# Kernel optimization log

Hardware: AMD Instinct MI355X
Metric: run time of the kernel (lower is better)

Reference implementation:

```python
import jax, jax.numpy as jnp
import numpy as np
from jax.scipy.special import gammaln

B, N, F, K = 128, 29, 64, 64
MAXZ, NITER, NPATH = 56, 2, 20
CUTOFF = 5.0


def setup_inputs() -> dict:
    key = jax.random.key(0)
    ks = jax.random.split(key, 16)
    atomic_numbers = jax.random.randint(ks[0], (B, N), 1, MAXZ)
    positions = jax.random.normal(ks[1], (B, N, 3), dtype=jnp.float32) * 2.0
    Ef = jax.random.normal(ks[2], (B, 3), dtype=jnp.float32)
    # fully connected molecular graph (all ordered pairs i != j), E = N*(N-1) = 812
    ii, jj = np.meshgrid(np.arange(N), np.arange(N), indexing="ij")
    m = ii != jj
    dst_idx = jnp.asarray(ii[m], dtype=jnp.int32)
    src_idx = jnp.asarray(jj[m], dtype=jnp.int32)
    s = 1.0 / np.sqrt(F)
    t = 0.2  # tensor-product path weight scale (keeps activations bounded)
    return {
        "atomic_numbers": atomic_numbers, "positions": positions, "Ef": Ef,
        "dst_idx": dst_idx, "src_idx": src_idx,
        "embed": jax.random.normal(ks[3], (MAXZ, F), dtype=jnp.float32) * s,
        "mp_basis_w": jax.random.normal(ks[4], (NITER, K, F), dtype=jnp.float32) / np.sqrt(K),
        "mp_tp_w": jax.random.normal(ks[5], (NITER, NPATH, F), dtype=jnp.float32) * t,
        "d1_w": jax.random.normal(ks[6], (NITER, 2, 2, F, F), dtype=jnp.float32) * s,
        "d1_b": jnp.zeros((NITER, 2, F), dtype=jnp.float32),
        "d2_w": jax.random.normal(ks[7], (NITER, 2, 2, F, F), dtype=jnp.float32) * s,
        "d2_b": jnp.zeros((NITER, 2, F), dtype=jnp.float32),
        "tens_w": jax.random.normal(ks[8], (NITER, NPATH, F), dtype=jnp.float32) * t,
        "td_dense_w": jax.random.normal(ks[9], (NITER, 2, 2, F, F), dtype=jnp.float32) * s,
        "td_tp_w": jax.random.normal(ks[10], (NITER, NPATH, F), dtype=jnp.float32) * t,
        "out_w": jax.random.normal(ks[11], (F,), dtype=jnp.float32) * s,
        "element_bias": jax.random.normal(ks[12], (MAXZ,), dtype=jnp.float32) * 0.1,
    }


def _tp(a, b, w):
    """Channelwise Clebsch-Gordan tensor product for max_degree=1 with parity channels.
    a, b: (M, 2, 4, F) with axis1 = (regular, pseudo), axis2 = (l=0, l=1 x/y/z).
    w: (20, F) learned per-path weights (5 l-paths x 4 parity combos)."""
    M, Fd = a.shape[0], a.shape[-1]
    sr = jnp.zeros((M, Fd), a.dtype); sp = jnp.zeros((M, Fd), a.dtype)
    vr = jnp.zeros((M, 3, Fd), a.dtype); vp = jnp.zeros((M, 3, Fd), a.dtype)
    idx = 0
    for p1 in range(2):
        for p2 in range(2):
            s1 = a[:, p1, 0]; v1 = a[:, p1, 1:4]
            s2 = b[:, p2, 0]; v2 = b[:, p2, 1:4]
            pl0a = 1 - 2 * p1; pl0b = 1 - 2 * p2   # parity of l=0 slot
            pl1a = -(1 - 2 * p1); pl1b = -(1 - 2 * p2)  # parity of l=1 slot
            tt = w[idx] * s1 * s2
            if pl0a * pl0b == 1: sr = sr + tt
            else: sp = sp + tt
            tt = w[idx + 1] * s1[:, None, :] * v2
            if pl0a * pl1b == -1: vr = vr + tt
            else: vp = vp + tt
            tt = w[idx + 2] * v1 * s2[:, None, :]
            if pl1a * pl0b == -1: vr = vr + tt
            else: vp = vp + tt
            tt = w[idx + 3] * jnp.sum(v1 * v2, axis=1)
            if pl1a * pl1b == 1: sr = sr + tt
            else: sp = sp + tt
            tt = w[idx + 4] * jnp.cross(v1, v2, axis=1)
            if pl1a * pl1b == -1: vr = vr + tt
            else: vp = vp + tt
            idx += 5
    reg = jnp.concatenate([sr[:, None, :], vr], axis=1)
    pse = jnp.concatenate([sp[:, None, :], vp], axis=1)
    return jnp.stack([reg, pse], axis=1)  # (M, 2, 4, F)


def _dense(x, W, b=None):
    # per-(parity, degree) linear map over features; W: (2, 2, F, F), b: (2, F)
    s = jnp.einsum("npf,pfg->npg", x[:, :, 0, :], W[:, 0])
    v = jnp.einsum("npdf,pfg->npdg", x[:, :, 1:4, :], W[:, 1])
    if b is not None:
        s = s + b
    return jnp.concatenate([s[:, :, None, :], v], axis=2)


def _silu(x):
    # gated equivariant silu: silu on scalars, sigmoid(scalar) gate on vectors
    s = x[:, :, 0:1, :]
    g = jax.nn.sigmoid(s)
    return jnp.concatenate([s * g, x[:, :, 1:4, :] * g], axis=2)


def _radial(r):
    # reciprocal Bernstein radial basis with smooth cutoff
    k = jnp.arange(K, dtype=r.dtype)
    logc = gammaln(float(K)) - gammaln(k + 1.0) - gammaln(float(K) - k)
    u = 1.0 / (1.0 + r)
    logb = logc + k * jnp.log(u)[:, None] + (K - 1.0 - k) * jnp.log(jnp.maximum(1.0 - u, 1e-12))[:, None]
    x2 = (r / CUTOFF) ** 2
    fcut = jnp.where(x2 < 1.0, jnp.exp(1.0 - 1.0 / jnp.maximum(1.0 - x2, 1e-12)), 0.0)
    return jnp.exp(logb) * fcut[:, None]  # (E, K)


def reference(atomic_numbers, positions, Ef, dst_idx, src_idx, embed, mp_basis_w,
              mp_tp_w, d1_w, d1_b, d2_w, d2_b, tens_w, td_dense_w, td_tp_w,
              out_w, element_bias):
    Bsz, Nn = atomic_numbers.shape
    BN = Bsz * Nn
    Fd = embed.shape[-1]
    pos = positions.reshape(-1, 3)
    Z = atomic_numbers.reshape(-1)
    offsets = (jnp.arange(Bsz, dtype=dst_idx.dtype) * Nn)
    dstf = (dst_idx[None, :] + offsets[:, None]).reshape(-1)  # (B*E,)
    srcf = (src_idx[None, :] + offsets[:, None]).reshape(-1)
    disp = pos[srcf] - pos[dstf]                               # (B*E, 3)
    r = jnp.sqrt(jnp.sum(disp * disp, axis=-1) + 1e-12)
    unit = disp / r[:, None]
    sph = jnp.concatenate([jnp.ones_like(r)[:, None], unit], axis=-1)  # (B*E, 4)
    basis = sph[:, :, None] * _radial(r)[:, None, :]           # (B*E, 4, K)

    x = jnp.zeros((BN, 2, 4, Fd), dtype=positions.dtype)
    x = x.at[:, 0, 0, :].set(embed[Z])

    xEFv = jnp.concatenate([jnp.ones((Bsz, 1), positions.dtype), Ef], axis=-1)  # (B, 4)
    xEF = jnp.repeat(xEFv, Nn, axis=0)                          # (BN, 4)
    xEF = jnp.broadcast_to(xEF[:, None, :, None], (BN, 2, 4, Fd))

    for i in range(NITER):
        bproj = jnp.einsum("edk,kf->edf", basis, mp_basis_w[i])  # (B*E, 4, F)
        bfeat = jnp.stack([bproj, jnp.zeros_like(bproj)], axis=1)  # (B*E, 2, 4, F)
        msg = _tp(x[srcf], bfeat, mp_tp_w[i])
        if i == NITER - 1:  # last iteration: max_degree=0 messages
            msg = msg * jnp.array([1.0, 0.0, 0.0, 0.0], msg.dtype)[None, None, :, None]
        y = jax.ops.segment_sum(msg, dstf, num_segments=BN)
        x = x + y
        h = _dense(x, d1_w[i], d1_b[i])
        h = _silu(h)
        h = _dense(h, d2_w[i], d2_b[i])
        x = h + y
        x = x + _tp(x, xEF, tens_w[i])          # Tensor()(x, xEF)
        x = _tp(x, _dense(x, td_dense_w[i]), td_tp_w[i])  # TensorDense

    s = x[:, 0, 0, :]  # degree-0 regular channel
    atomic_energies = s @ out_w + element_bias[Z]
    energy = atomic_energies.reshape(Bsz, Nn).sum(axis=1)
    return energy
```

## Files before the change

kernel.cpp:

```cpp
#include <hip/hip_runtime.h>

#define NB 128
#define NA 29
#define BN (NB*NA)
#define FD 64
#define RPLANE (BN*28*64)


__global__ void prep_kernel(const float* __restrict__ d1b,
                            const float* __restrict__ d2b,
                            const float* __restrict__ d2w,
                            float* __restrict__ logc, float* __restrict__ c4,
                            float* __restrict__ out)
{
  const int t = threadIdx.x;
  if (t < 64) {
    logc[t] = lgammaf(64.0f) - lgammaf((float)t + 1.0f) - lgammaf(64.0f - (float)t);
  } else if (t < 128) {
    const int g = t - 64;
    float acc = d2b[64 + g];
    for (int f = 0; f < 64; ++f) {
      const float v  = d1b[64 + f];
      const float sv = v / (1.0f + expf(-v));
      acc += d2w[2*4096 + f*64 + g] * sv;
    }
    c4[g] = acc;
  } else {
    out[t - 128] = 0.0f;
  }
}

__global__ __launch_bounds__(256, 3) void edge_rproj_kernel(
    const float* __restrict__ pos,
    const float* __restrict__ Wb,
    const float* __restrict__ logc_tab,
    float* __restrict__ rp)
{
  __shared__ float elu[28], el1mu[28], efc[28];
  __shared__ float rads[28][FD];
  const int bn = blockIdx.x, b = bn / NA, n = bn - b*NA;
  const int tid = threadIdx.x, lane = tid & 63, wv = tid >> 6;

  if (tid < 28) {
    const int jr = tid, j = jr + (jr >= n ? 1 : 0);
    const float dx = pos[(b*NA+j)*3+0] - pos[(b*NA+n)*3+0];
    const float dy = pos[(b*NA+j)*3+1] - pos[(b*NA+n)*3+1];
    const float dz = pos[(b*NA+j)*3+2] - pos[(b*NA+n)*3+2];
    const float r  = sqrtf(dx*dx + dy*dy + dz*dz + 1e-12f);
    const float u  = 1.0f/(1.0f + r);
    elu[jr]   = logf(u);
    el1mu[jr] = logf(fmaxf(1.0f - u, 1e-12f));
    const float x2 = (r*0.2f)*(r*0.2f);
    efc[jr] = (x2 < 1.0f) ? expf(1.0f - 1.0f/fmaxf(1.0f - x2, 1e-12f)) : 0.0f;
  }
  const float kk   = (float)lane;
  const float logc = logc_tab[lane];
  __syncthreads();

  #pragma unroll
  for (int i = 0; i < 7; ++i) {
    const int e = wv*7 + i;
    rads[e][lane] = expf(logc + kk*elu[e] + (63.0f - kk)*el1mu[e]) * efc[e];
  }
  float wb[64];
  #pragma unroll
  for (int k = 0; k < 64; ++k) wb[k] = Wb[k*FD + lane];

  #pragma unroll
  for (int i = 0; i < 7; ++i) {
    const int jr = wv*7 + i;
    float a0 = 0.0f;
    #pragma unroll
    for (int k4 = 0; k4 < 16; ++k4) {
      const float4 rv = *(const float4*)&rads[jr][k4*4];
      a0 += wb[k4*4+0]*rv.x + wb[k4*4+1]*rv.y + wb[k4*4+2]*rv.z + wb[k4*4+3]*rv.w;
    }
    rp[((size_t)bn*28 + jr)*64 + lane] = a0;
  }
}

__global__ __launch_bounds__(512) void msg0_kernel(
    const int*   __restrict__ Z,
    const float* __restrict__ pos,
    const float* __restrict__ embed,
    const float* __restrict__ wtp,
    const float* __restrict__ rp,
    float* __restrict__ y)
{
  __shared__ float emb_sh[NA][FD];
  __shared__ float posb[NA][3];
  __shared__ float us_sh[8][28][3];
  const int bi = blockIdx.x, b = bi >> 2, shard = bi & 3;
  const int tid = threadIdx.x, r = tid >> 6, g = tid & 63;

  if (tid < NA) {
    posb[tid][0] = pos[(b*NA+tid)*3+0];
    posb[tid][1] = pos[(b*NA+tid)*3+1];
    posb[tid][2] = pos[(b*NA+tid)*3+2];
  }
  __syncthreads();
  for (int idx = tid; idx < NA*FD; idx += 512)
    emb_sh[idx>>6][idx&63] = embed[Z[b*NA + (idx>>6)]*FD + (idx&63)];
  if (tid < 224) {
    const int rr = tid/28, jr = tid - rr*28, nn = shard*8 + rr;
    if (nn < NA) {
      const int j = jr + (jr >= nn ? 1 : 0);
      const float dx = posb[j][0]-posb[nn][0];
      const float dy = posb[j][1]-posb[nn][1];
      const float dz = posb[j][2]-posb[nn][2];
      const float ri = 1.0f / sqrtf(dx*dx + dy*dy + dz*dz + 1e-12f);
      us_sh[rr][jr][0] = dx*ri; us_sh[rr][jr][1] = dy*ri; us_sh[rr][jr][2] = dz*ri;
    }
  }
  __syncthreads();

  const int n = shard*8 + r;
  if (n >= NA) return;
  const int bn = b*NA + n;
  const float wm0 = wtp[0*FD + g], wm1 = wtp[1*FD + g];

  float rpa[28];
  {
    const float* rpb = rp + (size_t)bn*28*64 + g;
    #pragma unroll
    for (int jr = 0; jr < 28; ++jr) rpa[jr] = rpb[jr*64];
  }
  float y0 = 0.0f, y1 = 0.0f, y2 = 0.0f, y3 = 0.0f;
  #pragma unroll
  for (int jr = 0; jr < 28; ++jr) {
    const int j = jr + (jr >= n ? 1 : 0);
    const float t0 = rpa[jr] * emb_sh[j][g];
    y0 += wm0*t0;
    const float t1 = wm1*t0;
    y1 += t1*us_sh[r][jr][0];
    y2 += t1*us_sh[r][jr][1];
    y3 += t1*us_sh[r][jr][2];
  }
  float* yb = y + (size_t)bn*256 + g;
  yb[0] = y0; yb[64] = y1; yb[128] = y2; yb[192] = y3;
}

__global__ __launch_bounds__(512) void msg1_kernel(
    const float* __restrict__ pos,
    const float* __restrict__ wtp,
    const float* __restrict__ rp,
    const float* __restrict__ x,
    float* __restrict__ y)
{
  __shared__ float x_sh[NA][8][FD];
  __shared__ float posb[NA][3];
  __shared__ float us_sh[8][28][3];
  const int bi = blockIdx.x, b = bi >> 2, shard = bi & 3;
  const int tid = threadIdx.x, r = tid >> 6, g = tid & 63;

  if (tid < NA) {
    posb[tid][0] = pos[(b*NA+tid)*3+0];
    posb[tid][1] = pos[(b*NA+tid)*3+1];
    posb[tid][2] = pos[(b*NA+tid)*3+2];
  }
  __syncthreads();
  {
    float4* dst = (float4*)&x_sh[0][0][0];
    const float4* src = (const float4*)(x + (size_t)b*NA*512);
    for (int i = tid; i < NA*512/4; i += 512) dst[i] = src[i];
  }
  if (tid < 224) {
    const int rr = tid/28, jr = tid - rr*28, nn = shard*8 + rr;
    if (nn < NA) {
      const int j = jr + (jr >= nn ? 1 : 0);
      const float dx = posb[j][0]-posb[nn][0];
      const float dy = posb[j][1]-posb[nn][1];
      const float dz = posb[j][2]-posb[nn][2];
      const float ri = 1.0f / sqrtf(dx*dx + dy*dy + dz*dz + 1e-12f);
      us_sh[rr][jr][0] = dx*ri; us_sh[rr][jr][1] = dy*ri; us_sh[rr][jr][2] = dz*ri;
    }
  }
  __syncthreads();

  const int n = shard*8 + r;
  if (n >= NA) return;
  const int bn = b*NA + n;
  const float wm0 = wtp[0*FD+g], wm3 = wtp[3*FD+g];
  const float wm5 = wtp[10*FD+g], wm8 = wtp[13*FD+g];

  float rpa[28];
  {
    const float* rpb = rp + (size_t)bn*28*64 + g;
    #pragma unroll
    for (int jr = 0; jr < 28; ++jr) rpa[jr] = rpb[jr*64];
  }
  float y0 = 0.0f, y4 = 0.0f;
  #pragma unroll
  for (int jr = 0; jr < 28; ++jr) {
    const int j = jr + (jr >= n ? 1 : 0);
    const float ux = us_sh[r][jr][0], uy = us_sh[r][jr][1], uz = us_sh[r][jr][2];
    const float s1  = x_sh[j][0][g];
    const float dot1 = x_sh[j][1][g]*ux + x_sh[j][2][g]*uy + x_sh[j][3][g]*uz;
    const float s1p = x_sh[j][4][g];
    const float dotp = x_sh[j][5][g]*ux + x_sh[j][6][g]*uy + x_sh[j][7][g]*uz;
    y0 += rpa[jr]*(wm0*s1  + wm3*dot1);
    y4 += rpa[jr]*(wm5*s1p + wm8*dotp);
  }
  y[(size_t)bn*512 + g]       = y0;
  y[(size_t)bn*512 + 256 + g] = y4;
}

__device__ __forceinline__ void tp20(const float* a, const float* bb,
                                     const float* w, float* o)
{
  #pragma unroll
  for (int p1 = 0; p1 < 2; ++p1) {
    #pragma unroll
    for (int p2 = 0; p2 < 2; ++p2) {
      const float* w5 = w + 5*(2*p1 + p2);
      const float s1 = a[p1*4+0], x1 = a[p1*4+1], y1 = a[p1*4+2], z1 = a[p1*4+3];
      const float s2 = bb[p2*4+0], x2 = bb[p2*4+1], y2 = bb[p2*4+2], z2 = bb[p2*4+3];
      const int so = (p1 == p2) ? 0 : 4;
      const int vo = 4 - so;
      o[so+0] += w5[0]*(s1*s2) + w5[3]*(x1*x2 + y1*y2 + z1*z2);
      o[so+1] += w5[1]*(s1*x2) + w5[2]*(x1*s2);
      o[so+2] += w5[1]*(s1*y2) + w5[2]*(y1*s2);
      o[so+3] += w5[1]*(s1*z2) + w5[2]*(z1*s2);
      o[vo+1] += w5[4]*(y1*z2 - z1*y2);
      o[vo+2] += w5[4]*(z1*x2 - x1*z2);
      o[vo+3] += w5[4]*(x1*y2 - y1*x2);
    }
  }
}

__device__ __forceinline__ void stage2(float* __restrict__ wst,
                                       const float* __restrict__ src, int tid)
{
  const float4* s = (const float4*)src;
  float4* d = (float4*)wst;
  #pragma unroll
  for (int i = 0; i < 8; ++i) d[tid + i*256] = s[tid + i*256];
}

__device__ __forceinline__ void denseP2(const float* __restrict__ wst,
                                        const float* __restrict__ rA,
                                        const float* __restrict__ rB,
                                        float bs, int g,
                                        float oA[4], float oB[4])
{
  float a0A = bs, a0B = bs;
  #pragma unroll
  for (int f4 = 0; f4 < 16; ++f4) {
    const float w0 = wst[(f4*4+0)*64+g], w1 = wst[(f4*4+1)*64+g];
    const float w2 = wst[(f4*4+2)*64+g], w3 = wst[(f4*4+3)*64+g];
    const float4 xA = *(const float4*)&rA[f4*4];
    const float4 xB = *(const float4*)&rB[f4*4];
    a0A += w0*xA.x + w1*xA.y + w2*xA.z + w3*xA.w;
    a0B += w0*xB.x + w1*xB.y + w2*xB.z + w3*xB.w;
  }
  oA[0] = a0A; oB[0] = a0B;
  float a1A = 0, a2A = 0, a3A = 0, a1B = 0, a2B = 0, a3B = 0;
  #pragma unroll
  for (int f4 = 0; f4 < 16; ++f4) {
    const float w0 = wst[4096+(f4*4+0)*64+g], w1 = wst[4096+(f4*4+1)*64+g];
    const float w2 = wst[4096+(f4*4+2)*64+g], w3 = wst[4096+(f4*4+3)*64+g];
    const float4 aA = *(const float4*)&rA[ 64+f4*4];
    const float4 bA = *(const float4*)&rA[128+f4*4];
    const float4 cA = *(const float4*)&rA[192+f4*4];
    const float4 aB = *(const float4*)&rB[ 64+f4*4];
    const float4 bB = *(const float4*)&rB[128+f4*4];
    const float4 cB = *(const float4*)&rB[192+f4*4];
    a1A += w0*aA.x + w1*aA.y + w2*aA.z + w3*aA.w;
    a2A += w0*bA.x + w1*bA.y + w2*bA.z + w3*bA.w;
    a3A += w0*cA.x + w1*cA.y + w2*cA.z + w3*cA.w;
    a1B += w0*aB.x + w1*aB.y + w2*aB.z + w3*aB.w;
    a2B += w0*bB.x + w1*bB.y + w2*bB.z + w3*bB.w;
    a3B += w0*cB.x + w1*cB.y + w2*cB.z + w3*cB.w;
  }
  oA[1] = a1A; oA[2] = a2A; oA[3] = a3A;
  oB[1] = a1B; oB[2] = a2B; oB[3] = a3B;
}

template<bool LAST>
__global__ __launch_bounds__(256) void node_kernel(
    const int*   __restrict__ Z,
    const float* __restrict__ embed,
    const float* __restrict__ Ef,
    const float* __restrict__ d1w, const float* __restrict__ d1b,
    const float* __restrict__ d2w, const float* __restrict__ d2b,
    const float* __restrict__ tens_w,
    const float* __restrict__ tdw,
    const float* __restrict__ td_tp_w,
    const float* __restrict__ out_w,
    const float* __restrict__ ebias,
    const float* __restrict__ c4,
    const float* __restrict__ xin,
    const float* __restrict__ yin,
    float* __restrict__ xout,
    float* __restrict__ out)
{
  __shared__ float wst[2*64*64];
  __shared__ float row[8][8][FD];
  const int tid = threadIdx.x, r = tid >> 6, g = tid & 63;
  const int ndA = blockIdx.x*8 + r*2, ndB = ndA + 1;
  float* rowA = &row[r*2+0][0][0];
  float* rowB = &row[r*2+1][0][0];

  float yA[4], yB[4];
  float y0A = 0, y4A = 0, y0B = 0, y4B = 0;
  if constexpr (!LAST) {
    #pragma unroll
    for (int c = 0; c < 4; ++c) {
      yA[c] = yin[(size_t)ndA*256 + c*64 + g];
      yB[c] = yin[(size_t)ndB*256 + c*64 + g];
    }
    rowA[g] = embed[Z[ndA]*FD + g] + yA[0];
    rowB[g] = embed[Z[ndB]*FD + g] + yB[0];
    #pragma unroll
    for (int c = 1; c < 4; ++c) { rowA[c*64+g] = yA[c]; rowB[c*64+g] = yB[c]; }
  } else {
    y0A = yin[(size_t)ndA*512 + g];     y4A = yin[(size_t)ndA*512 + 256 + g];
    y0B = yin[(size_t)ndB*512 + g];     y4B = yin[(size_t)ndB*512 + 256 + g];
    #pragma unroll
    for (int pc = 0; pc < 8; ++pc) {
      float vA = xin[(size_t)ndA*512 + pc*64 + g];
      float vB = xin[(size_t)ndB*512 + pc*64 + g];
      if (pc == 0) { vA += y0A; vB += y0B; }
      if (pc == 4) { vA += y4A; vB += y4B; }
      rowA[pc*64+g] = vA; rowB[pc*64+g] = vB;
    }
  }
  stage2(wst, d1w, tid);
  __syncthreads();

  {
    float hA[4], hB[4];
    denseP2(wst, rowA, rowB, d1b[g], g, hA, hB);
    const float sA = 1.0f/(1.0f + expf(-hA[0]));
    const float sB = 1.0f/(1.0f + expf(-hB[0]));
    rowA[g] = hA[0]*sA; rowB[g] = hB[0]*sB;
    #pragma unroll
    for (int c = 1; c < 4; ++c) { rowA[c*64+g] = hA[c]*sA; rowB[c*64+g] = hB[c]*sB; }
  }
  __syncthreads();
  if constexpr (LAST) {
    stage2(wst, d1w + 8192, tid);
    __syncthreads();
    float hA[4], hB[4];
    denseP2(wst, rowA + 256, rowB + 256, d1b[64+g], g, hA, hB);
    const float sA = 1.0f/(1.0f + expf(-hA[0]));
    const float sB = 1.0f/(1.0f + expf(-hB[0]));
    rowA[256+g] = hA[0]*sA; rowB[256+g] = hB[0]*sB;
    #pragma unroll
    for (int c = 1; c < 4; ++c) { rowA[256+c*64+g] = hA[c]*sA; rowB[256+c*64+g] = hB[c]*sB; }
    __syncthreads();
  }
  stage2(wst, d2w, tid);
  __syncthreads();

  float x2A[8], x2B[8];
  {
    float oA[4], oB[4];
    denseP2(wst, rowA, rowB, d2b[g], g, oA, oB);
    #pragma unroll
    for (int c = 0; c < 4; ++c) { x2A[c] = oA[c]; x2B[c] = oB[c]; }
  }
  if constexpr (!LAST) {
    #pragma unroll
    for (int c = 0; c < 4; ++c) { x2A[c] += yA[c]; x2B[c] += yB[c]; }
    const float c4v = c4[g];
    x2A[4] = c4v; x2B[4] = c4v;
    x2A[5] = x2A[6] = x2A[7] = 0.0f;
    x2B[5] = x2B[6] = x2B[7] = 0.0f;
  } else {
    x2A[0] += y0A; x2B[0] += y0B;
    __syncthreads();
    stage2(wst, d2w + 8192, tid);
    __syncthreads();
    float oA[4], oB[4];
    denseP2(wst, rowA + 256, rowB + 256, d2b[64+g], g, oA, oB);
    x2A[4] = oA[0] + y4A; x2A[5] = oA[1]; x2A[6] = oA[2]; x2A[7] = oA[3];
    x2B[4] = oB[0] + y4B; x2B[5] = oB[1]; x2B[6] = oB[2]; x2B[7] = oB[3];
  }

  float x3A[8], x3B[8];
  {
    float w20[20];
    #pragma unroll
    for (int q = 0; q < 20; ++q) w20[q] = tens_w[q*FD + g];
    const int bA = ndA / NA, bB = ndB / NA;
    {
      const float bbv[8] = {1.0f, Ef[bA*3+0], Ef[bA*3+1], Ef[bA*3+2],
                            1.0f, Ef[bA*3+0], Ef[bA*3+1], Ef[bA*3+2]};
      float o[8] = {0,0,0,0,0,0,0,0};
      tp20(x2A, bbv, w20, o);
      #pragma unroll
      for (int pc = 0; pc < 8; ++pc) { x3A[pc] = x2A[pc] + o[pc]; rowA[pc*64+g] = x3A[pc]; }
    }
    {
      const float bbv[8] = {1.0f, Ef[bB*3+0], Ef[bB*3+1], Ef[bB*3+2],
                            1.0f, Ef[bB*3+0], Ef[bB*3+1], Ef[bB*3+2]};
      float o[8] = {0,0,0,0,0,0,0,0};
      tp20(x2B, bbv, w20, o);
      #pragma unroll
      for (int pc = 0; pc < 8; ++pc) { x3B[pc] = x2B[pc] + o[pc]; rowB[pc*64+g] = x3B[pc]; }
    }
  }
  __syncthreads();
  stage2(wst, tdw, tid);
  __syncthreads();

  float tdA[8], tdB[8];
  {
    float oA[4], oB[4];
    denseP2(wst, rowA, rowB, 0.0f, g, oA, oB);
    #pragma unroll
    for (int c = 0; c < 4; ++c) { tdA[c] = oA[c]; tdB[c] = oB[c]; }
  }
  __syncthreads();
  stage2(wst, tdw + 8192, tid);
  __syncthreads();
  {
    float oA[4], oB[4];
    denseP2(wst, rowA + 256, rowB + 256, 0.0f, g, oA, oB);
    #pragma unroll
    for (int c = 0; c < 4; ++c) { tdA[4+c] = oA[c]; tdB[4+c] = oB[c]; }
  }

  if constexpr (LAST) {
    const float wa = td_tp_w[0*FD+g],  wb = td_tp_w[3*FD+g];
    const float wc = td_tp_w[15*FD+g], wd = td_tp_w[18*FD+g];
    const float ow = out_w[g];
    float pA = ow * (wa*(x3A[0]*tdA[0])
                   + wb*(x3A[1]*tdA[1] + x3A[2]*tdA[2] + x3A[3]*tdA[3])
                   + wc*(x3A[4]*tdA[4])
                   + wd*(x3A[5]*tdA[5] + x3A[6]*tdA[6] + x3A[7]*tdA[7]));
    float pB = ow * (wa*(x3B[0]*tdB[0])
                   + wb*(x3B[1]*tdB[1] + x3B[2]*tdB[2] + x3B[3]*tdB[3])
                   + wc*(x3B[4]*tdB[4])
                   + wd*(x3B[5]*tdB[5] + x3B[6]*tdB[6] + x3B[7]*tdB[7]));
    #pragma unroll
    for (int off = 32; off > 0; off >>= 1) {
      pA += __shfl_xor(pA, off, 64);
      pB += __shfl_xor(pB, off, 64);
    }
    if (g == 0) {
      atomicAdd(&out[ndA/NA], pA + ebias[Z[ndA]]);
      atomicAdd(&out[ndB/NA], pB + ebias[Z[ndB]]);
    }
  } else {
    float w20[20];
    #pragma unroll
    for (int q = 0; q < 20; ++q) w20[q] = td_tp_w[q*FD + g];
    {
      float o[8] = {0,0,0,0,0,0,0,0};
      tp20(x3A, tdA, w20, o);
      #pragma unroll
      for (int pc = 0; pc < 8; ++pc) xout[(size_t)ndA*512 + pc*64 + g] = o[pc];
    }
    {
      float o[8] = {0,0,0,0,0,0,0,0};
      tp20(x3B, tdB, w20, o);
      #pragma unroll
      for (int pc = 0; pc < 8; ++pc) xout[(size_t)ndB*512 + pc*64 + g] = o[pc];
    }
  }
}

extern "C" void kernel_launch(void* const* d_in, const int* in_sizes, int n_in,
                              void* d_out, int out_size, void* d_ws, size_t ws_size,
                              hipStream_t stream)
{
  (void)in_sizes; (void)n_in; (void)out_size; (void)ws_size;
  const int*   Z     = (const int*)  d_in[0];
  const float* pos   = (const float*)d_in[1];
  const float* Ef    = (const float*)d_in[2];
  const float* embed = (const float*)d_in[5];
  const float* mpbw  = (const float*)d_in[6];
  const float* mptpw = (const float*)d_in[7];
  const float* d1w   = (const float*)d_in[8];
  const float* d1b   = (const float*)d_in[9];
  const float* d2w   = (const float*)d_in[10];
  const float* d2b   = (const float*)d_in[11];
  const float* tensw = (const float*)d_in[12];
  const float* tdw   = (const float*)d_in[13];
  const float* tdtpw = (const float*)d_in[14];
  const float* outw  = (const float*)d_in[15];
  const float* ebias = (const float*)d_in[16];
  float* out = (float*)d_out;

  float* logc = (float*)d_ws;
  float* c4   = logc + 64;
  float* rpT  = c4 + 64;
  float* xg   = rpT + RPLANE;
  float* yg   = xg + (size_t)BN*512;

  prep_kernel<<<1, 256, 0, stream>>>(d1b, d2b, d2w, logc, c4, out);
  edge_rproj_kernel<<<BN, 256, 0, stream>>>(pos, mpbw, logc, rpT);
  msg0_kernel<<<NB*4, 512, 0, stream>>>(Z, pos, embed, mptpw, rpT, yg);
  node_kernel<false><<<BN/8, 256, 0, stream>>>(Z, embed, Ef,
      d1w, d1b, d2w, d2b, tensw, tdw, tdtpw, outw, ebias, c4,
      nullptr, yg, xg, nullptr);
  edge_rproj_kernel<<<BN, 256, 0, stream>>>(pos, mpbw + 4096, logc, rpT);
  msg1_kernel<<<NB*4, 512, 0, stream>>>(pos, mptpw + 1280, rpT, xg, yg);
  node_kernel<true><<<BN/8, 256, 0, stream>>>(Z, embed, Ef,
      d1w + 16384, d1b + 128, d2w + 16384, d2b + 128, tensw + 1280,
      tdw + 16384, tdtpw + 1280, outw, ebias, c4,
      xg, yg, nullptr, out);
}
```

Before: 141.0 us.

## Fuse radial projection into message kernels to drop the rp intermediate buffer

Merges edge_rproj_kernel with msg0/msg1 into one templated fmsg_kernel per node. The radial projection result is consumed directly in registers, so the BN*28*64 rp plane is never written to or read from global memory, and two launches are removed. Unit vectors are computed in the same block, and per-wave partial sums are reduced through shared memory. In exchange, the embedding gather runs per node block instead of per batch shard, and in the LAST variant neighbor x values are read from global memory rather than staged in shared memory.

Result: faster. 124.4 us (-11.8%).

```diff
diff --git a/kernel.cpp b/kernel.cpp
--- a/kernel.cpp
+++ b/kernel.cpp
@@ -4,7 +4,6 @@
 #define NA 29
 #define BN (NB*NA)
 #define FD 64
-#define RPLANE (BN*28*64)
 
 
 __global__ void prep_kernel(const float* __restrict__ d1b,
@@ -30,14 +29,21 @@
   }
 }
 
-__global__ __launch_bounds__(256, 3) void edge_rproj_kernel(
+template<bool LAST>
+__global__ __launch_bounds__(256) void fmsg_kernel(
+    const int*   __restrict__ Z,
     const float* __restrict__ pos,
+    const float* __restrict__ src,
+    const float* __restrict__ wtp,
     const float* __restrict__ Wb,
     const float* __restrict__ logc_tab,
-    float* __restrict__ rp)
+    float* __restrict__ y)
 {
   __shared__ float elu[28], el1mu[28], efc[28];
+  __shared__ float us[28][3];
   __shared__ float rads[28][FD];
+  __shared__ float emb_sh[NA][FD];
+  __shared__ float yred[4][4][FD];
   const int bn = blockIdx.x, b = bn / NA, n = bn - b*NA;
   const int tid = threadIdx.x, lane = tid & 63, wv = tid >> 6;
 
@@ -47,12 +53,18 @@
     const float dy = pos[(b*NA+j)*3+1] - pos[(b*NA+n)*3+1];
     const float dz = pos[(b*NA+j)*3+2] - pos[(b*NA+n)*3+2];
     const float r  = sqrtf(dx*dx + dy*dy + dz*dz + 1e-12f);
+    const float ri = 1.0f / r;
+    us[jr][0] = dx*ri; us[jr][1] = dy*ri; us[jr][2] = dz*ri;
     const float u  = 1.0f/(1.0f + r);
     elu[jr]   = logf(u);
     el1mu[jr] = logf(fmaxf(1.0f - u, 1e-12f));
     const float x2 = (r*0.2f)*(r*0.2f);
     efc[jr] = (x2 < 1.0f) ? expf(1.0f - 1.0f/fmaxf(1.0f - x2, 1e-12f)) : 0.0f;
   }
+  if constexpr (!LAST) {
+    for (int idx = tid; idx < NA*FD; idx += 256)
+      emb_sh[idx>>6][idx&63] = src[Z[b*NA + (idx>>6)]*FD + (idx&63)];
+  }
   const float kk   = (float)lane;
   const float logc = logc_tab[lane];
   __syncthreads();
@@ -66,6 +78,13 @@
   #pragma unroll
   for (int k = 0; k < 64; ++k) wb[k] = Wb[k*FD + lane];
 
+  float y0 = 0.0f, y1 = 0.0f, y2 = 0.0f, y3 = 0.0f, y4 = 0.0f;
+  const float wm0 = wtp[0*FD + lane];
+  const float wm1 = LAST ? 0.0f : wtp[1*FD + lane];
+  const float wm3 = LAST ? wtp[3*FD + lane]  : 0.0f;
+  const float wm5 = LAST ? wtp[10*FD + lane] : 0.0f;
+  const float wm8 = LAST ? wtp[13*FD + lane] : 0.0f;
+
   #pragma unroll
   for (int i = 0; i < 7; ++i) {
     const int jr = wv*7 + i;
@@ -75,134 +94,48 @@
       const float4 rv = *(const float4*)&rads[jr][k4*4];
       a0 += wb[k4*4+0]*rv.x + wb[k4*4+1]*rv.y + wb[k4*4+2]*rv.z + wb[k4*4+3]*rv.w;
     }
-    rp[((size_t)bn*28 + jr)*64 + lane] = a0;
-  }
-}
-
-__global__ __launch_bounds__(512) void msg0_kernel(
-    const int*   __restrict__ Z,
-    const float* __restrict__ pos,
-    const float* __restrict__ embed,
-    const float* __restrict__ wtp,
-    const float* __restrict__ rp,
-    float* __restrict__ y)
-{
-  __shared__ float emb_sh[NA][FD];
-  __shared__ float posb[NA][3];
-  __shared__ float us_sh[8][28][3];
-  const int bi = blockIdx.x, b = bi >> 2, shard = bi & 3;
-  const int tid = threadIdx.x, r = tid >> 6, g = tid & 63;
-
-  if (tid < NA) {
-    posb[tid][0] = pos[(b*NA+tid)*3+0];
-    posb[tid][1] = pos[(b*NA+tid)*3+1];
-    posb[tid][2] = pos[(b*NA+tid)*3+2];
-  }
-  __syncthreads();
-  for (int idx = tid; idx < NA*FD; idx += 512)
-    emb_sh[idx>>6][idx&63] = embed[Z[b*NA + (idx>>6)]*FD + (idx&63)];
-  if (tid < 224) {
-    const int rr = tid/28, jr = tid - rr*28, nn = shard*8 + rr;
-    if (nn < NA) {
-      const int j = jr + (jr >= nn ? 1 : 0);
-      const float dx = posb[j][0]-posb[nn][0];
-      const float dy = posb[j][1]-posb[nn][1];
-      const float dz = posb[j][2]-posb[nn][2];
-      const float ri = 1.0f / sqrtf(dx*dx + dy*dy + dz*dz + 1e-12f);
-      us_sh[rr][jr][0] = dx*ri; us_sh[rr][jr][1] = dy*ri; us_sh[rr][jr][2] = dz*ri;
-    }
-  }
-  __syncthreads();
-
-  const int n = shard*8 + r;
-  if (n >= NA) return;
-  const int bn = b*NA + n;
-  const float wm0 = wtp[0*FD + g], wm1 = wtp[1*FD + g];
-
-  float rpa[28];
-  {
-    const float* rpb = rp + (size_t)bn*28*64 + g;
-    #pragma unroll
-    for (int jr = 0; jr < 28; ++jr) rpa[jr] = rpb[jr*64];
-  }
-  float y0 = 0.0f, y1 = 0.0f, y2 = 0.0f, y3 = 0.0f;
-  #pragma unroll
-  for (int jr = 0; jr < 28; ++jr) {
     const int j = jr + (jr >= n ? 1 : 0);
-    const float t0 = rpa[jr] * emb_sh[j][g];
-    y0 += wm0*t0;
-    const float t1 = wm1*t0;
-    y1 += t1*us_sh[r][jr][0];
-    y2 += t1*us_sh[r][jr][1];
-    y3 += t1*us_sh[r][jr][2];
-  }
-  float* yb = y + (size_t)bn*256 + g;
-  yb[0] = y0; yb[64] = y1; yb[128] = y2; yb[192] = y3;
-}
-
-__global__ __launch_bounds__(512) void msg1_kernel(
-    const float* __restrict__ pos,
-    const float* __restrict__ wtp,
-    const float* __restrict__ rp,
-    const float* __restrict__ x,
-    float* __restrict__ y)
-{
-  __shared__ float x_sh[NA][8][FD];
-  __shared__ float posb[NA][3];
-  __shared__ float us_sh[8][28][3];
-  const int bi = blockIdx.x, b = bi >> 2, shard = bi & 3;
-  const int tid = threadIdx.x, r = tid >> 6, g = tid & 63;
-
-  if (tid < NA) {
-    posb[tid][0] = pos[(b*NA+tid)*3+0];
-    posb[tid][1] = pos[(b*NA+tid)*3+1];
-    posb[tid][2] = pos[(b*NA+tid)*3+2];
-  }
-  __syncthreads();
-  {
-    float4* dst = (float4*)&x_sh[0][0][0];
-    const float4* src = (const float4*)(x + (size_t)b*NA*512);
-    for (int i = tid; i < NA*512/4; i += 512) dst[i] = src[i];
-  }
-  if (tid < 224) {
-    const int rr = tid/28, jr = tid - rr*28, nn = shard*8 + rr;
-    if (nn < NA) {
-      const int j = jr + (jr >= nn ? 1 : 0);
-      const float dx = posb[j][0]-posb[nn][0];
-      const float dy = posb[j][1]-posb[nn][1];
-      const float dz = posb[j][2]-posb[nn][2];
-      const float ri = 1.0f / sqrtf(dx*dx + dy*dy + dz*dz + 1e-12f);
-      us_sh[rr][jr][0] = dx*ri; us_sh[rr][jr][1] = dy*ri; us_sh[rr][jr][2] = dz*ri;
-    }
-  }
-  __syncthreads();
-
-  const int n = shard*8 + r;
-  if (n >= NA) return;
-  const int bn = b*NA + n;
-  const float wm0 = wtp[0*FD+g], wm3 = wtp[3*FD+g];
-  const float wm5 = wtp[10*FD+g], wm8 = wtp[13*FD+g];
-
-  float rpa[28];
-  {
-    const float* rpb = rp + (size_t)bn*28*64 + g;
-    #pragma unroll
-    for (int jr = 0; jr < 28; ++jr) rpa[jr] = rpb[jr*64];
-  }
-  float y0 = 0.0f, y4 = 0.0f;
-  #pragma unroll
-  for (int jr = 0; jr < 28; ++jr) {
-    const int j = jr + (jr >= n ? 1 : 0);
-    const float ux = us_sh[r][jr][0], uy = us_sh[r][jr][1], uz = us_sh[r][jr][2];
-    const float s1  = x_sh[j][0][g];
-    const float dot1 = x_sh[j][1][g]*ux + x_sh[j][2][g]*uy + x_sh[j][3][g]*uz;
-    const float s1p = x_sh[j][4][g];
-    const float dotp = x_sh[j][5][g]*ux + x_sh[j][6][g]*uy + x_sh[j][7][g]*uz;
-    y0 += rpa[jr]*(wm0*s1  + wm3*dot1);
-    y4 += rpa[jr]*(wm5*s1p + wm8*dotp);
-  }
-  y[(size_t)bn*512 + g]       = y0;
-  y[(size_t)bn*512 + 256 + g] = y4;
+    const float ux = us[jr][0], uy = us[jr][1], uz = us[jr][2];
+    if constexpr (!LAST) {
+      const float t0 = a0 * emb_sh[j][lane];
+      y0 += wm0*t0;
+      const float t1 = wm1*t0;
+      y1 += t1*ux; y2 += t1*uy; y3 += t1*uz;
+    } else {
+      const float* xj = src + (size_t)(b*NA + j)*512 + lane;
+      const float s1   = xj[0];
+      const float dot1 = xj[64]*ux + xj[128]*uy + xj[192]*uz;
+      const float s1p  = xj[256];
+      const float dotp = xj[320]*ux + xj[384]*uy + xj[448]*uz;
+      y0 += a0*(wm0*s1  + wm3*dot1);
+      y4 += a0*(wm5*s1p + wm8*dotp);
+    }
+  }
+
+  if constexpr (!LAST) {
+    yred[wv][0][lane] = y0; yred[wv][1][lane] = y1;
+    yred[wv][2][lane] = y2; yred[wv][3][lane] = y3;
+  } else {
+    yred[wv][0][lane] = y0; yred[wv][1][lane] = y4;
+  }
+  __syncthreads();
+  if (wv == 0) {
+    if constexpr (!LAST) {
+      #pragma unroll
+      for (int c = 0; c < 4; ++c) {
+        const float s = yred[0][c][lane] + yred[1][c][lane]
+                      + yred[2][c][lane] + yred[3][c][lane];
+        y[(size_t)bn*256 + c*64 + lane] = s;
+      }
+    } else {
+      const float s0 = yred[0][0][lane] + yred[1][0][lane]
+                     + yred[2][0][lane] + yred[3][0][lane];
+      const float s4 = yred[0][1][lane] + yred[1][1][lane]
+                     + yred[2][1][lane] + yred[3][1][lane];
+      y[(size_t)bn*512 + lane]       = s0;
+      y[(size_t)bn*512 + 256 + lane] = s4;
+    }
+  }
 }
 
 __device__ __forceinline__ void tp20(const float* a, const float* bb,
@@ -486,18 +419,16 @@
 
   float* logc = (float*)d_ws;
   float* c4   = logc + 64;
-  float* rpT  = c4 + 64;
-  float* xg   = rpT + RPLANE;
+  float* xg   = c4 + 64;
   float* yg   = xg + (size_t)BN*512;
 
   prep_kernel<<<1, 256, 0, stream>>>(d1b, d2b, d2w, logc, c4, out);
-  edge_rproj_kernel<<<BN, 256, 0, stream>>>(pos, mpbw, logc, rpT);
-  msg0_kernel<<<NB*4, 512, 0, stream>>>(Z, pos, embed, mptpw, rpT, yg);
+  fmsg_kernel<false><<<BN, 256, 0, stream>>>(Z, pos, embed, mptpw, mpbw, logc, yg);
   node_kernel<false><<<BN/8, 256, 0, stream>>>(Z, embed, Ef,
       d1w, d1b, d2w, d2b, tensw, tdw, tdtpw, outw, ebias, c4,
       nullptr, yg, xg, nullptr);
-  edge_rproj_kernel<<<BN, 256, 0, stream>>>(pos, mpbw + 4096, logc, rpT);
-  msg1_kernel<<<NB*4, 512, 0, stream>>>(pos, mptpw + 1280, rpT, xg, yg);
+  fmsg_kernel<true><<<BN, 256, 0, stream>>>(Z, pos, xg, mptpw + 1280,
+      mpbw + 4096, logc, yg);
   node_kernel<true><<<BN/8, 256, 0, stream>>>(Z, embed, Ef,
       d1w + 16384, d1b + 128, d2w + 16384, d2b + 128, tensw + 1280,
       tdw + 16384, tdtpw + 1280, outw, ebias, c4,
```
